# Optimization experiments

Measured on AMD Instinct MI355X. Metric: run time of the kernel, lower is better.

## Reference

```python
import jax, jax.numpy as jnp
import numpy as np

B, C, H, W = 32, 2048, 24, 24
P, RED = 4, 16


def setup_inputs() -> dict:
    key = jax.random.key(0)
    ks = jax.random.split(key, 7)
    return {
        "x": jax.random.normal(ks[0], (B, C, H, W), dtype=jnp.float32),
        "fc1_w": jax.random.normal(ks[1], (C // RED, C), dtype=jnp.float32) * 0.02,
        "fc1_b": jax.random.normal(ks[2], (C // RED,), dtype=jnp.float32) * 0.02,
        "fc2_w": jax.random.normal(ks[3], (C * P, C // RED), dtype=jnp.float32) * 0.02,
        "fc2_b": jax.random.normal(ks[4], (C * P,), dtype=jnp.float32) * 0.02,
        "conv_w": jax.random.normal(ks[5], (C,), dtype=jnp.float32) * 0.02,
        "conv_b": jax.random.normal(ks[6], (C,), dtype=jnp.float32) * 0.02,
    }


def reference(x, fc1_w, fc1_b, fc2_w, fc2_b, conv_w, conv_b):
    # SE-style dynamic weight generation
    pooled = x.mean(axis=(2, 3))                                  # (B, C)
    hidden = jax.nn.silu(pooled @ fc1_w.T + fc1_b)                # (B, C//red)
    dw = (hidden @ fc2_w.T + fc2_b).reshape(B, P, C)              # (B, P, C)
    # depthwise 1x1 conv == per-channel scale + bias
    base = x * conv_w[None, :, None, None] + conv_b[None, :, None, None]
    # per-part channel-weighted reduction: out[b,p,h,w] = sum_c base[b,c,h,w]*dw[b,p,c]
    out = jnp.einsum('bchw,bpc->bphw', base, dw)                  # (B, P, H, W)
    return jax.nn.softmax(out, axis=1)
```

## Files before the change

### kernel.cpp

```cpp
#include <hip/hip_runtime.h>
#include <hip/hip_bf16.h>
#include <math.h>

#define B_ 32
#define C_ 2048
#define HW_ 576
#define P_ 4
#define HID_ 128
#define J_ 8192
#define NCHUNK_ 16
#define NSLOT_ 64

__global__ void pool_kernel(const float* __restrict__ x, float* __restrict__ pooled) {
    int gwave = blockIdx.x * 4 + (threadIdx.x >> 6);
    int lane  = threadIdx.x & 63;
    const float4* xp4 = (const float4*)(x + (size_t)gwave * HW_);
    float s = 0.f;
    for (int i = lane; i < HW_ / 4; i += 64) {
        float4 v = xp4[i];
        s += v.x + v.y + v.z + v.w;
    }
    #pragma unroll
    for (int off = 32; off > 0; off >>= 1) s += __shfl_down(s, off, 64);
    if (lane == 0) pooled[gwave] = s * (1.0f / (float)HW_);
}

__global__ void fc1_trans_kernel(const float* __restrict__ pooled, const float* __restrict__ fc1_w,
                                 const float* __restrict__ fc1_b, float* __restrict__ hidden,
                                 const float* __restrict__ fc2_w, float* __restrict__ wt) {
    int bid = blockIdx.x;
    int tid = threadIdx.x;
    if (bid < 1024) {
        int o    = bid * 4 + (tid >> 6);
        int lane = tid & 63;
        int b = o >> 7;
        int j = o & 127;
        const float* pr = pooled + (size_t)b * C_;
        const float* wr = fc1_w + (size_t)j * C_;
        float s = 0.f;
        for (int k = lane; k < C_; k += 64) s += pr[k] * wr[k];
        #pragma unroll
        for (int off = 32; off > 0; off >>= 1) s += __shfl_down(s, off, 64);
        if (lane == 0) {
            float z = s + fc1_b[j];
            hidden[o] = z / (1.0f + expf(-z));
        }
    } else {
        __shared__ float tile[32][33];
        int bid2 = bid - 1024;
        int kt = bid2 & 3;
        int jt = bid2 >> 2;
        int tx = tid & 31;
        int ty = tid >> 5;
        #pragma unroll
        for (int i = 0; i < 32; i += 8)
            tile[ty + i][tx] = fc2_w[(size_t)(jt * 32 + ty + i) * HID_ + kt * 32 + tx];
        __syncthreads();
        #pragma unroll
        for (int i = 0; i < 32; i += 8)
            wt[(size_t)(kt * 32 + ty + i) * J_ + jt * 32 + tx] = tile[tx][ty + i];
    }
}

__global__ void fc2_kernel(const float* __restrict__ hidden, const float* __restrict__ wt,
                           const float* __restrict__ bias, float* __restrict__ dw) {
    int b  = blockIdx.x >> 3;
    int jc = blockIdx.x & 7;
    int tid = threadIdx.x;

    __shared__ float h[HID_];
    if (tid < HID_) h[tid] = hidden[(size_t)b * HID_ + tid];
    __syncthreads();

    int j4 = jc * 256 + tid;
    const float4* wt4 = (const float4*)wt;
    float4 acc = {0.f, 0.f, 0.f, 0.f};
    #pragma unroll 8
    for (int k = 0; k < HID_; ++k) {
        float4 wv = wt4[(size_t)k * (J_ / 4) + j4];
        float hk = h[k];
        acc.x += wv.x * hk;
        acc.y += wv.y * hk;
        acc.z += wv.z * hk;
        acc.w += wv.w * hk;
    }
    const float4* b4 = (const float4*)bias;
    float4 bb = b4[j4];
    acc.x += bb.x; acc.y += bb.y; acc.z += bb.z; acc.w += bb.w;
    ((float4*)(dw + (size_t)b * J_))[j4] = acc;
}

__global__ void biasc_kernel(const float* __restrict__ conv_b, const float* __restrict__ dw,
                             float* __restrict__ bias_const) {
    int o    = blockIdx.x * 4 + (threadIdx.x >> 6);
    int lane = threadIdx.x & 63;
    const float* dr = dw + (size_t)o * C_;
    float s = 0.f;
    for (int k = lane; k < C_; k += 64) s += conv_b[k] * dr[k];
    #pragma unroll
    for (int off = 32; off > 0; off >>= 1) s += __shfl_down(s, off, 64);
    if (lane == 0) bias_const[o] = s;
}

__global__ void einsum_kernel(const float* __restrict__ x, const float* __restrict__ conv_w,
                              const float* __restrict__ dw, float* __restrict__ part) {
    int b     = blockIdx.x;
    int chunk = blockIdx.y;
    int c0    = chunk * 128;
    int tid   = threadIdx.x;

    __shared__ float4 m4[128];
    if (tid < 128) {
        float cw = conv_w[c0 + tid];
        const float* dr = dw + (size_t)b * (P_ * C_) + c0 + tid;
        float4 v;
        v.x = cw * dr[0 * C_];
        v.y = cw * dr[1 * C_];
        v.z = cw * dr[2 * C_];
        v.w = cw * dr[3 * C_];
        m4[tid] = v;
    }
    __syncthreads();

    int g = tid / 144;
    int i = tid - g * 144;

    float4 a0 = {0,0,0,0}, a1 = {0,0,0,0}, a2 = {0,0,0,0}, a3 = {0,0,0,0};
    const float* xb = x + ((size_t)b * C_ + c0) * HW_;
    #pragma unroll 4
    for (int k = 0; k < 32; ++k) {
        int c = g + 4 * k;
        float4 v = ((const float4*)(xb + (size_t)c * HW_))[i];
        float4 m = m4[c];
        a0.x += v.x * m.x; a0.y += v.y * m.x; a0.z += v.z * m.x; a0.w += v.w * m.x;
        a1.x += v.x * m.y; a1.y += v.y * m.y; a1.z += v.z * m.y; a1.w += v.w * m.y;
        a2.x += v.x * m.z; a2.y += v.y * m.z; a2.z += v.z * m.z; a2.w += v.w * m.z;
        a3.x += v.x * m.w; a3.y += v.y * m.w; a3.z += v.z * m.w; a3.w += v.w * m.w;
    }
    int slot = chunk * 4 + g;
    float4* pp = (float4*)(part + (((size_t)b * NSLOT_ + slot) * P_) * HW_) + i;
    pp[0 * (HW_ / 4)] = a0;
    pp[1 * (HW_ / 4)] = a1;
    pp[2 * (HW_ / 4)] = a2;
    pp[3 * (HW_ / 4)] = a3;
}

__global__ void softmax_kernel(const float* __restrict__ part, const float* __restrict__ bias_const,
                               float* __restrict__ out) {
    int idx = blockIdx.x * 256 + threadIdx.x;
    int b  = idx / HW_;
    int hw = idx - b * HW_;
    const float* bc = bias_const + b * P_;
    float v0 = bc[0], v1 = bc[1], v2 = bc[2], v3 = bc[3];
    const float* pb = part + ((size_t)b * NSLOT_ * P_) * HW_ + hw;
    #pragma unroll 8
    for (int s = 0; s < NSLOT_; ++s) {
        const float* ps = pb + (size_t)s * P_ * HW_;
        v0 += ps[0 * HW_];
        v1 += ps[1 * HW_];
        v2 += ps[2 * HW_];
        v3 += ps[3 * HW_];
    }
    float mx = fmaxf(fmaxf(v0, v1), fmaxf(v2, v3));
    float e0 = expf(v0 - mx), e1 = expf(v1 - mx), e2 = expf(v2 - mx), e3 = expf(v3 - mx);
    float inv = 1.0f / (e0 + e1 + e2 + e3);
    float* op = out + ((size_t)b * P_) * HW_ + hw;
    op[0 * HW_] = e0 * inv;
    op[1 * HW_] = e1 * inv;
    op[2 * HW_] = e2 * inv;
    op[3 * HW_] = e3 * inv;
}

extern "C" void kernel_launch(void* const* d_in, const int* in_sizes, int n_in,
                              void* d_out, int out_size, void* d_ws, size_t ws_size,
                              hipStream_t stream) {
    const float* x      = (const float*)d_in[0];
    const float* fc1_w  = (const float*)d_in[1];
    const float* fc1_b  = (const float*)d_in[2];
    const float* fc2_w  = (const float*)d_in[3];
    const float* fc2_b  = (const float*)d_in[4];
    const float* conv_w = (const float*)d_in[5];
    const float* conv_b = (const float*)d_in[6];
    float* out = (float*)d_out;

    float* ws      = (float*)d_ws;
    float* pooled  = ws;
    float* hidden  = pooled + 65536;
    float* dw      = hidden + 4096;
    float* bias_c  = dw + 262144;
    float* part    = bias_c + 128;
    float* wt      = part + 4718592;

    pool_kernel<<<16384, 256, 0, stream>>>(x, pooled);
    fc1_trans_kernel<<<2048, 256, 0, stream>>>(pooled, fc1_w, fc1_b, hidden, fc2_w, wt);
    fc2_kernel<<<256, 256, 0, stream>>>(hidden, wt, fc2_b, dw);
    biasc_kernel<<<32, 256, 0, stream>>>(conv_b, dw, bias_c);
    einsum_kernel<<<dim3(B_, NCHUNK_), 576, 0, stream>>>(x, conv_w, dw, part);
    softmax_kernel<<<72, 256, 0, stream>>>(part, bias_c, out);
}
```

Measured before the change: 287.6 us.

## Reduce einsum partials in shared memory and fuse bias reduction into fc2

The einsum kernel now handles 256 channels per block and sums its four channel-group partials in shared memory before writing. This cuts the partial-sum buffer and the softmax reads by a factor of eight. The conv-bias dot product is moved into the fc2 epilogue as per-block partials, which removes one kernel launch. The tradeoff is half as many einsum blocks and extra shared memory plus a sync per block, which may reduce latency hiding while streaming x.

```diff
diff --git a/kernel.cpp b/kernel.cpp
--- a/kernel.cpp
+++ b/kernel.cpp
@@ -8,8 +8,8 @@
 #define P_ 4
 #define HID_ 128
 #define J_ 8192
-#define NCHUNK_ 16
-#define NSLOT_ 64
+#define NCHUNK_ 8
+#define NSLOT_ 8
 
 __global__ void pool_kernel(const float* __restrict__ x, float* __restrict__ pooled) {
     int gwave = blockIdx.x * 4 + (threadIdx.x >> 6);
@@ -63,7 +63,8 @@
 }
 
 __global__ void fc2_kernel(const float* __restrict__ hidden, const float* __restrict__ wt,
-                           const float* __restrict__ bias, float* __restrict__ dw) {
+                           const float* __restrict__ bias, const float* __restrict__ conv_b,
+                           float* __restrict__ dw, float* __restrict__ bias_part) {
     int b  = blockIdx.x >> 3;
     int jc = blockIdx.x & 7;
     int tid = threadIdx.x;
@@ -88,29 +89,28 @@
     float4 bb = b4[j4];
     acc.x += bb.x; acc.y += bb.y; acc.z += bb.z; acc.w += bb.w;
     ((float4*)(dw + (size_t)b * J_))[j4] = acc;
-}
-
-__global__ void biasc_kernel(const float* __restrict__ conv_b, const float* __restrict__ dw,
-                             float* __restrict__ bias_const) {
-    int o    = blockIdx.x * 4 + (threadIdx.x >> 6);
-    int lane = threadIdx.x & 63;
-    const float* dr = dw + (size_t)o * C_;
-    float s = 0.f;
-    for (int k = lane; k < C_; k += 64) s += conv_b[k] * dr[k];
+
+    int c = (4 * j4) & (C_ - 1);
+    float4 cb = *(const float4*)(conv_b + c);
+    float local = cb.x * acc.x + cb.y * acc.y + cb.z * acc.z + cb.w * acc.w;
     #pragma unroll
-    for (int off = 32; off > 0; off >>= 1) s += __shfl_down(s, off, 64);
-    if (lane == 0) bias_const[o] = s;
+    for (int off = 32; off > 0; off >>= 1) local += __shfl_down(local, off, 64);
+    __shared__ float wsum[4];
+    if ((tid & 63) == 0) wsum[tid >> 6] = local;
+    __syncthreads();
+    if (tid == 0) bias_part[(b << 3) + jc] = wsum[0] + wsum[1] + wsum[2] + wsum[3];
 }
 
 __global__ void einsum_kernel(const float* __restrict__ x, const float* __restrict__ conv_w,
                               const float* __restrict__ dw, float* __restrict__ part) {
     int b     = blockIdx.x;
     int chunk = blockIdx.y;
-    int c0    = chunk * 128;
+    int c0    = chunk * 256;
     int tid   = threadIdx.x;
 
-    __shared__ float4 m4[128];
-    if (tid < 128) {
+    __shared__ float4 m4[256];
+    __shared__ float4 red[P_ * HW_];
+    if (tid < 256) {
         float cw = conv_w[c0 + tid];
         const float* dr = dw + (size_t)b * (P_ * C_) + c0 + tid;
         float4 v;
@@ -128,7 +128,7 @@
     float4 a0 = {0,0,0,0}, a1 = {0,0,0,0}, a2 = {0,0,0,0}, a3 = {0,0,0,0};
     const float* xb = x + ((size_t)b * C_ + c0) * HW_;
     #pragma unroll 4
-    for (int k = 0; k < 32; ++k) {
+    for (int k = 0; k < 64; ++k) {
         int c = g + 4 * k;
         float4 v = ((const float4*)(xb + (size_t)c * HW_))[i];
         float4 m = m4[c];
@@ -137,23 +137,41 @@
         a2.x += v.x * m.z; a2.y += v.y * m.z; a2.z += v.z * m.z; a2.w += v.w * m.z;
         a3.x += v.x * m.w; a3.y += v.y * m.w; a3.z += v.z * m.w; a3.w += v.w * m.w;
     }
-    int slot = chunk * 4 + g;
-    float4* pp = (float4*)(part + (((size_t)b * NSLOT_ + slot) * P_) * HW_) + i;
-    pp[0 * (HW_ / 4)] = a0;
-    pp[1 * (HW_ / 4)] = a1;
-    pp[2 * (HW_ / 4)] = a2;
-    pp[3 * (HW_ / 4)] = a3;
-}
-
-__global__ void softmax_kernel(const float* __restrict__ part, const float* __restrict__ bias_const,
+    red[0 * HW_ + tid] = a0;
+    red[1 * HW_ + tid] = a1;
+    red[2 * HW_ + tid] = a2;
+    red[3 * HW_ + tid] = a3;
+    __syncthreads();
+
+    if (g == 0) {
+        float4* pp = (float4*)(part + (((size_t)b * NSLOT_ + chunk) * P_) * HW_);
+        #pragma unroll
+        for (int p = 0; p < P_; ++p) {
+            float4 s  = red[p * HW_ + i];
+            float4 s1 = red[p * HW_ + 144 + i];
+            float4 s2 = red[p * HW_ + 288 + i];
+            float4 s3 = red[p * HW_ + 432 + i];
+            s.x += s1.x + s2.x + s3.x;
+            s.y += s1.y + s2.y + s3.y;
+            s.z += s1.z + s2.z + s3.z;
+            s.w += s1.w + s2.w + s3.w;
+            pp[p * (HW_ / 4) + i] = s;
+        }
+    }
+}
+
+__global__ void softmax_kernel(const float* __restrict__ part, const float* __restrict__ bias_part,
                                float* __restrict__ out) {
     int idx = blockIdx.x * 256 + threadIdx.x;
     int b  = idx / HW_;
     int hw = idx - b * HW_;
-    const float* bc = bias_const + b * P_;
-    float v0 = bc[0], v1 = bc[1], v2 = bc[2], v3 = bc[3];
+    const float* bp = bias_part + b * 8;
+    float v0 = bp[0] + bp[1];
+    float v1 = bp[2] + bp[3];
+    float v2 = bp[4] + bp[5];
+    float v3 = bp[6] + bp[7];
     const float* pb = part + ((size_t)b * NSLOT_ * P_) * HW_ + hw;
-    #pragma unroll 8
+    #pragma unroll
     for (int s = 0; s < NSLOT_; ++s) {
         const float* ps = pb + (size_t)s * P_ * HW_;
         v0 += ps[0 * HW_];
@@ -183,18 +201,17 @@
     const float* conv_b = (const float*)d_in[6];
     float* out = (float*)d_out;
 
-    float* ws      = (float*)d_ws;
-    float* pooled  = ws;
-    float* hidden  = pooled + 65536;
-    float* dw      = hidden + 4096;
-    float* bias_c  = dw + 262144;
-    float* part    = bias_c + 128;
-    float* wt      = part + 4718592;
+    float* ws        = (float*)d_ws;
+    float* pooled    = ws;
+    float* hidden    = pooled + 65536;
+    float* dw        = hidden + 4096;
+    float* bias_part = dw + 262144;
+    float* part      = bias_part + 256;
+    float* wt        = part + 589824;
 
     pool_kernel<<<16384, 256, 0, stream>>>(x, pooled);
     fc1_trans_kernel<<<2048, 256, 0, stream>>>(pooled, fc1_w, fc1_b, hidden, fc2_w, wt);
-    fc2_kernel<<<256, 256, 0, stream>>>(hidden, wt, fc2_b, dw);
-    biasc_kernel<<<32, 256, 0, stream>>>(conv_b, dw, bias_c);
+    fc2_kernel<<<256, 256, 0, stream>>>(hidden, wt, fc2_b, conv_b, dw, bias_part);
     einsum_kernel<<<dim3(B_, NCHUNK_), 576, 0, stream>>>(x, conv_w, dw, part);
-    softmax_kernel<<<72, 256, 0, stream>>>(part, bias_c, out);
-}
+    softmax_kernel<<<72, 256, 0, stream>>>(part, bias_part, out);
+}
```

New measurement: 269.6 us. 1.07x faster.
